# Optimization experiments

Measured on AMD Instinct MI355X. Metric: run time of the kernel, lower is better.

Reference implementation:

```python
import jax, jax.numpy as jnp
import numpy as np

B = 2048          # number of tables (real batch size)
C = 8             # columns per table
D = 768           # hidden size (BERT-base)
TEMP = 0.07       # hp.temp
NEG_FILL = -10.0


def setup_inputs() -> dict:
    key = jax.random.key(0)
    k1, k2, k3 = jax.random.split(key, 3)
    n = B * C
    z = jax.random.normal(k1, (2 * n, D), jnp.float32) * 0.05
    idx = jnp.repeat(jnp.arange(B, dtype=jnp.int32), C)  # contiguous segment ids, as torch.full per table
    query = jax.random.normal(k2, (D, 1), jnp.float32) * 0.05
    attn_temp = jnp.ones((), jnp.float32)
    W = jax.random.normal(k3, (D, D), jnp.float32) * 0.02
    b = jnp.zeros((D,), jnp.float32)
    return {"z": z, "ori_table_indices": idx, "aug_table_indices": idx,
            "query": query, "attn_temp": attn_temp, "W": W, "b": b}


def _attn_pool(z, idx, query, t):
    # scatter-softmax attention pooling over variable-size table segments
    scores = (z @ query)[:, 0] / t                               # [n]
    e = jnp.exp(scores - scores.max())
    denom = jax.ops.segment_sum(e, idx, num_segments=B)[idx]     # [n]
    w = e / (denom + 1e-8)
    return jax.ops.segment_sum(z * w[:, None], idx, num_segments=B)  # [B, D]


def reference(z, ori_table_indices, aug_table_indices, query, attn_temp, W, b):
    n = B * C
    z_ori, z_aug = z[:n], z[n:]
    gx = _attn_pool(z_ori, ori_table_indices, query, attn_temp) @ W.T + b  # [B, D]
    hx = _attn_pool(z_aug, aug_table_indices, query, attn_temp) @ W.T + b  # [B, D]
    f = jnp.concatenate([gx, hx], axis=0)                                  # [2B, D]
    f = f / jnp.linalg.norm(f, axis=1, keepdims=True)
    sim = f @ f.T                                                          # [2B, 2B]
    N = 2 * B
    lab = jnp.concatenate([jnp.arange(B), jnp.arange(B)])
    labels = lab[None, :] == lab[:, None]                                  # [N, N] bool
    potential_pos = (sim > 0.9) & (~labels)
    safe_neg = (~potential_pos) & (~labels)
    # remove diagonal via rotation gather (order of negatives is irrelevant: topk sorts)
    cols = (jnp.arange(N)[:, None] + jnp.arange(1, N)[None, :]) % N        # [N, N-1]
    sim_od = jnp.take_along_axis(sim, cols, axis=1)
    safe_od = jnp.take_along_axis(safe_neg, cols, axis=1)
    # each row's single positive is its paired view at column (i+B) mod N
    pos = jnp.take_along_axis(sim, ((jnp.arange(N) + B) % N)[:, None], axis=1)  # [N, 1]
    neg = jnp.where(safe_od, sim_od, NEG_FILL)
    # data-dependent k; static-shape topk via descending sort + column mask
    k = jnp.maximum(1, jnp.floor(0.5 * jnp.mean(jnp.sum(safe_od, axis=1).astype(jnp.float32))).astype(jnp.int32))
    sneg = -jnp.sort(-neg, axis=1)                                         # descending
    new_neg = jnp.where(jnp.arange(N - 1)[None, :] < k, sneg, NEG_FILL)
    logits = jnp.concatenate([pos, new_neg], axis=1) / TEMP                # [N, N]
    # cross-entropy with target class 0
    loss = jnp.mean(jax.nn.logsumexp(logits, axis=1) - logits[:, 0])
    return loss
```

## Files before the change

kernel.cpp:

```cpp
#include <hip/hip_runtime.h>
#include <hip/hip_bf16.h>
#include <math.h>

#define Bq   2048
#define Cq   8
#define Dq   768
#define NROW 16384
#define NTOT 32768
#define Nq   4096
#define TEMPq 0.07f

typedef __attribute__((ext_vector_type(8))) short bf16x8;
typedef __attribute__((ext_vector_type(4))) float f32x4;
typedef __attribute__((ext_vector_type(8))) _Float16 f16x8;
typedef __attribute__((ext_vector_type(4))) _Float16 f16x4;

__device__ __hip_bfloat16 g_pooledb[(size_t)Nq * Dq];
__device__ __hip_bfloat16 g_Wb[(size_t)Dq * Dq];
__device__ float          g_f[(size_t)Nq * Dq];
__device__ __hip_bfloat16 g_fb[(size_t)Nq * Dq];
__device__ _Float16       g_simh[(size_t)Nq * Nq];
__device__ unsigned int   g_viol;
__device__ float          g_rowloss[Nq];

#define GLDS16(src, dst) __builtin_amdgcn_global_load_lds( \
    (const __attribute__((address_space(1))) void*)(src),  \
    (__attribute__((address_space(3))) void*)(dst), 16, 0, 0)

__global__ __launch_bounds__(256) void prep_kernel(const float* __restrict__ z,
                                                   const float* __restrict__ query,
                                                   const float* __restrict__ attn_temp,
                                                   const float* __restrict__ W) {
    if (blockIdx.x >= 1024) {
        int i = (blockIdx.x - 1024) * 256 + threadIdx.x;
        if (i == 0) g_viol = 0u;
        float4 v = ((const float4*)W)[i];
        short4 o;
        o.x = ((__hip_bfloat16_raw)__float2bfloat16(v.x)).x;
        o.y = ((__hip_bfloat16_raw)__float2bfloat16(v.y)).x;
        o.z = ((__hip_bfloat16_raw)__float2bfloat16(v.z)).x;
        o.w = ((__hip_bfloat16_raw)__float2bfloat16(v.w)).x;
        ((short4*)g_Wb)[i] = o;
        return;
    }
    int seg  = (int)((blockIdx.x * blockDim.x + threadIdx.x) >> 6);
    int lane = threadIdx.x & 63;
    if (seg >= Nq) return;
    int half = seg >> 11;
    int b    = seg & 2047;
    int baseRow = half * NROW + b * Cq;
    float invt = 1.f / attn_temp[0];

    float4 q4[3];
#pragma unroll
    for (int j = 0; j < 3; ++j) q4[j] = *(const float4*)(query + j * 256 + lane * 4);

    float4 v4[Cq][3];
    float s[Cq];
#pragma unroll
    for (int c = 0; c < Cq; ++c) {
        const float* zr = z + (size_t)(baseRow + c) * Dq;
        float acc = 0.f;
#pragma unroll
        for (int j = 0; j < 3; ++j) {
            float4 vz = *(const float4*)(zr + j * 256 + lane * 4);
            v4[c][j] = vz;
            acc += vz.x * q4[j].x + vz.y * q4[j].y + vz.z * q4[j].z + vz.w * q4[j].w;
        }
#pragma unroll
        for (int o = 32; o > 0; o >>= 1) acc += __shfl_xor(acc, o, 64);
        s[c] = acc * invt;
    }
    float m = s[0];
#pragma unroll
    for (int c = 1; c < Cq; ++c) m = fmaxf(m, s[c]);
    float e[Cq], denom = 0.f;
#pragma unroll
    for (int c = 0; c < Cq; ++c) { e[c] = expf(s[c] - m); denom += e[c]; }
    float inv = 1.f / (denom + 1e-8f);
#pragma unroll
    for (int j = 0; j < 3; ++j) {
        float4 acc = {0.f, 0.f, 0.f, 0.f};
#pragma unroll
        for (int c = 0; c < Cq; ++c) {
            acc.x += v4[c][j].x * e[c];
            acc.y += v4[c][j].y * e[c];
            acc.z += v4[c][j].z * e[c];
            acc.w += v4[c][j].w * e[c];
        }
        short4 o;
        o.x = ((__hip_bfloat16_raw)__float2bfloat16(acc.x * inv)).x;
        o.y = ((__hip_bfloat16_raw)__float2bfloat16(acc.y * inv)).x;
        o.z = ((__hip_bfloat16_raw)__float2bfloat16(acc.z * inv)).x;
        o.w = ((__hip_bfloat16_raw)__float2bfloat16(acc.w * inv)).x;
        *(short4*)((short*)g_pooledb + (size_t)seg * Dq + j * 256 + lane * 4) = o;
    }
}

__global__ __launch_bounds__(256) void fw_mfma_kernel(const float* __restrict__ bias) {
    __shared__ short lA[128 * 32];
    __shared__ short lB[128 * 32];
    const int bm = blockIdx.y * 128;
    const int bn = blockIdx.x * 128;

    const int tid  = threadIdx.x;
    const int wave = tid >> 6, lane = tid & 63;
    const int wr = wave >> 1, wc = wave & 1;

    const short* A = (const short*)g_pooledb;
    const short* Bt = (const short*)g_Wb;

    const int c0 = wave * 2, c1 = wave * 2 + 1;
    const int srow = lane >> 2;
    const int scol = (lane & 3) * 8;

    f32x4 acc[4][4];
#pragma unroll
    for (int m = 0; m < 4; ++m)
#pragma unroll
        for (int n = 0; n < 4; ++n) acc[m][n] = (f32x4){0.f, 0.f, 0.f, 0.f};

    for (int k0 = 0; k0 < Dq; k0 += 32) {
        GLDS16(A  + (size_t)(bm + c0 * 16 + srow) * Dq + k0 + scol, lA + c0 * 512);
        GLDS16(A  + (size_t)(bm + c1 * 16 + srow) * Dq + k0 + scol, lA + c1 * 512);
        GLDS16(Bt + (size_t)(bn + c0 * 16 + srow) * Dq + k0 + scol, lB + c0 * 512);
        GLDS16(Bt + (size_t)(bn + c1 * 16 + srow) * Dq + k0 + scol, lB + c1 * 512);
        __syncthreads();

        bf16x8 af[4], bfr[4];
#pragma unroll
        for (int m = 0; m < 4; ++m) {
            int row = wr * 64 + m * 16 + (lane & 15);
            af[m] = *(const bf16x8*)(lA + row * 32 + (lane >> 4) * 8);
        }
#pragma unroll
        for (int n = 0; n < 4; ++n) {
            int row = wc * 64 + n * 16 + (lane & 15);
            bfr[n] = *(const bf16x8*)(lB + row * 32 + (lane >> 4) * 8);
        }
#pragma unroll
        for (int m = 0; m < 4; ++m)
#pragma unroll
            for (int n = 0; n < 4; ++n)
                acc[m][n] = __builtin_amdgcn_mfma_f32_16x16x32_bf16(af[m], bfr[n], acc[m][n], 0, 0, 0);
        __syncthreads();
    }

#pragma unroll
    for (int m = 0; m < 4; ++m) {
        int rowb = bm + wr * 64 + m * 16 + (lane >> 4) * 4;
#pragma unroll
        for (int n = 0; n < 4; ++n) {
            int col = bn + wc * 64 + n * 16 + (lane & 15);
            float bc = bias[col];
#pragma unroll
            for (int j = 0; j < 4; ++j)
                g_f[(size_t)(rowb + j) * Dq + col] = acc[m][n][j] + bc;
        }
    }
}

__global__ __launch_bounds__(256) void normalize_kernel() {
    int row  = (int)((blockIdx.x * blockDim.x + threadIdx.x) >> 6);
    int lane = threadIdx.x & 63;
    if (row >= Nq) return;
    float ss = 0.f;
    float v[Dq / 64];
#pragma unroll
    for (int j = 0; j < Dq / 64; ++j) { v[j] = g_f[(size_t)row * Dq + j * 64 + lane]; ss += v[j] * v[j]; }
#pragma unroll
    for (int o = 32; o > 0; o >>= 1) ss += __shfl_xor(ss, o, 64);
    float rn = 1.f / sqrtf(ss);
#pragma unroll
    for (int j = 0; j < Dq / 64; ++j)
        g_fb[(size_t)row * Dq + j * 64 + lane] = __float2bfloat16(v[j] * rn);
}

__global__ __launch_bounds__(256) void sim_mfma_kernel() {
    __shared__ short lA[128 * 32];
    __shared__ short lB[128 * 32];

    int t = blockIdx.x;
    int bi = 0, rem = t;
    while (rem >= (32 - bi)) { rem -= (32 - bi); ++bi; }
    int bj = bi + rem;
    int bm = bi * 128, bn = bj * 128;

    const int tid  = threadIdx.x;
    const int wave = tid >> 6, lane = tid & 63;
    const int wr = wave >> 1, wc = wave & 1;

    const short* fb = (const short*)g_fb;

    const int c0 = wave * 2, c1 = wave * 2 + 1;
    const int srow = lane >> 2;
    const int scol = (lane & 3) * 8;

    f32x4 acc[4][4];
#pragma unroll
    for (int m = 0; m < 4; ++m)
#pragma unroll
        for (int n = 0; n < 4; ++n) acc[m][n] = (f32x4){0.f, 0.f, 0.f, 0.f};

    for (int k0 = 0; k0 < Dq; k0 += 32) {
        GLDS16(fb + (size_t)(bm + c0 * 16 + srow) * Dq + k0 + scol, lA + c0 * 512);
        GLDS16(fb + (size_t)(bm + c1 * 16 + srow) * Dq + k0 + scol, lA + c1 * 512);
        GLDS16(fb + (size_t)(bn + c0 * 16 + srow) * Dq + k0 + scol, lB + c0 * 512);
        GLDS16(fb + (size_t)(bn + c1 * 16 + srow) * Dq + k0 + scol, lB + c1 * 512);
        __syncthreads();

        bf16x8 af[4], bfr[4];
#pragma unroll
        for (int m = 0; m < 4; ++m) {
            int row = wr * 64 + m * 16 + (lane & 15);
            af[m] = *(const bf16x8*)(lA + row * 32 + (lane >> 4) * 8);
        }
#pragma unroll
        for (int n = 0; n < 4; ++n) {
            int row = wc * 64 + n * 16 + (lane & 15);
            bfr[n] = *(const bf16x8*)(lB + row * 32 + (lane >> 4) * 8);
        }
#pragma unroll
        for (int m = 0; m < 4; ++m)
#pragma unroll
            for (int n = 0; n < 4; ++n)
                acc[m][n] = __builtin_amdgcn_mfma_f32_16x16x32_bf16(af[m], bfr[n], acc[m][n], 0, 0, 0);
        __syncthreads();
    }

    int vio = 0;
#pragma unroll
    for (int m = 0; m < 4; ++m) {
        int rowb = bm + wr * 64 + m * 16 + (lane >> 4) * 4;
#pragma unroll
        for (int n = 0; n < 4; ++n) {
            int col = bn + wc * 64 + n * 16 + (lane & 15);
#pragma unroll
            for (int j = 0; j < 4; ++j) {
                g_simh[(size_t)(rowb + j) * Nq + col] = (_Float16)acc[m][n][j];
                vio += (acc[m][n][j] > 0.9f) && ((((rowb + j) ^ col) & 2047) != 0);
            }
        }
    }
    if (bi != bj) {
#pragma unroll
        for (int m = 0; m < 4; ++m) {
            int rowb = bm + wr * 64 + m * 16 + (lane >> 4) * 4;
#pragma unroll
            for (int n = 0; n < 4; ++n) {
                int col = bn + wc * 64 + n * 16 + (lane & 15);
                f16x4 h;
#pragma unroll
                for (int j = 0; j < 4; ++j) h[j] = (_Float16)acc[m][n][j];
                *(f16x4*)&g_simh[(size_t)col * Nq + rowb] = h;
            }
        }
        vio *= 2;
    }
#pragma unroll
    for (int o = 32; o > 0; o >>= 1) vio += __shfl_xor(vio, o, 64);
    if (lane == 0 && vio > 0) atomicAdd(&g_viol, (unsigned int)vio);
}

__global__ __launch_bounds__(256) void lse_kernel() {
    const int row_id = (int)((blockIdx.x * blockDim.x + threadIdx.x) >> 6);
    const int lane = threadIdx.x & 63;
    const _Float16* row = g_simh + (size_t)row_id * Nq;
    const int labi = row_id & 2047;
    const float invT = 1.0f / TEMPq;

    long long total = (long long)Nq * 4094LL - (long long)g_viol;
    int k = (int)(total / 8192LL);
    if (k < 1) k = 1;

    float v[64];
    float mx = -1e30f, mn = 1e30f;
    int cnt = 0;
#pragma unroll
    for (int q = 0; q < 8; ++q) {
        int j0 = q * 512 + lane * 8;
        f16x8 x8 = *(const f16x8*)(row + j0);
#pragma unroll
        for (int s = 0; s < 8; ++s) {
            int jj = q * 8 + s;
            int j  = j0 + s;
            float xv = (float)x8[s];
            bool sf = (xv <= 0.9f) && (((j ^ labi) & 2047) != 0);
            float val = sf ? xv : -2.0f;
            v[jj] = val;
            mx = fmaxf(mx, val);
            mn = fminf(mn, sf ? xv : 2.0f);
            cnt += (int)__popcll(__ballot(sf));
        }
    }
#pragma unroll
    for (int o = 32; o > 0; o >>= 1) {
        mx = fmaxf(mx, __shfl_xor(mx, o, 64));
        mn = fminf(mn, __shfl_xor(mn, o, 64));
    }

    const float pos = (float)row[(row_id + Bq) & (Nq - 1)];
    const float mxs = (cnt > 0) ? mx : -10.0f;
    const float ml  = fmaxf(pos, mxs) * invT;

    float lo = mn - 1e-3f, hi = mx;
    int c_hi = 0;
    const bool need = (cnt > k);
    if (need) {
        for (int it = 0; it < 12; ++it) {
            float mid = 0.5f * (lo + hi);
            int c = 0;
#pragma unroll
            for (int jj = 0; jj < 64; ++jj)
                c += (int)__popcll(__ballot(v[jj] > mid));
            if (c > k) lo = mid; else { hi = mid; c_hi = c; }
        }
    }

    float shi = 0.f, st = 0.f; int nt = 0;
#pragma unroll
    for (int jj = 0; jj < 64; ++jj) {
        float x = v[jj];
        float ev = __expf(x * invT - ml);
        if (!need)       { if (x > -1.5f) shi += ev; }
        else if (x > hi) { shi += ev; }
        else if (x > lo) { st += ev; nt++; }
    }
#pragma unroll
    for (int o = 32; o > 0; o >>= 1) {
        shi += __shfl_xor(shi, o, 64);
        st  += __shfl_xor(st,  o, 64);
        nt  += __shfl_xor(nt,  o, 64);
    }
    if (lane == 0) {
        float S = __expf(pos * invT - ml) + shi;
        if (need && c_hi < k && nt > 0)
            S += st * (float)(k - c_hi) / (float)nt;
        g_rowloss[row_id] = (logf(S) + ml) - pos * invT;
    }
}

__global__ __launch_bounds__(256) void loss_kernel(float* __restrict__ out) {
    float s = 0.f;
    for (int i = threadIdx.x; i < Nq; i += 256) s += g_rowloss[i];
    __shared__ float sm[256];
    sm[threadIdx.x] = s; __syncthreads();
    for (int o = 128; o > 0; o >>= 1) {
        if (threadIdx.x < o) sm[threadIdx.x] += sm[threadIdx.x + o];
        __syncthreads();
    }
    if (threadIdx.x == 0) out[0] = sm[0] / (float)Nq;
}

extern "C" void kernel_launch(void* const* d_in, const int* in_sizes, int n_in,
                              void* d_out, int out_size, void* d_ws, size_t ws_size,
                              hipStream_t stream) {
    const float* z         = (const float*)d_in[0];
    const float* query     = (const float*)d_in[3];
    const float* attn_temp = (const float*)d_in[4];
    const float* W         = (const float*)d_in[5];
    const float* bias      = (const float*)d_in[6];
    float* out = (float*)d_out;

    prep_kernel<<<1024 + (Dq * Dq / 4) / 256, 256, 0, stream>>>(z, query, attn_temp, W);
    fw_mfma_kernel<<<dim3(Dq / 128, Nq / 128), 256, 0, stream>>>(bias);
    normalize_kernel<<<Nq / 4, 256, 0, stream>>>();
    sim_mfma_kernel<<<(32 * 33) / 2, 256, 0, stream>>>();
    lse_kernel<<<Nq / 4, 256, 0, stream>>>();
    loss_kernel<<<1, 256, 0, stream>>>(out);
}
```

Baseline: 121.3 us.

## Retile sim GEMM to 256x256 double-buffered tiles with k-chunked operand layout

The normalize kernel now writes the normalized bf16 features in a k-chunk-major layout (8-element chunks, row-contiguous within each chunk) so the similarity GEMM can stage tiles with fully coalesced direct-to-LDS loads. The similarity kernel moves from 128x128 upper-triangle tiles with 256 threads to a full 16x16 grid of 256x256 tiles with 512 threads, double-buffered LDS (128KB) and explicit vmcnt waits, so the next tile's loads overlap the MFMAs. It drops the symmetric transposed write-back and computes the whole matrix, which doubles the MFMA work. In return it gains larger per-block reuse, better load overlap and fully coalesced stores.

```diff
diff --git a/kernel.cpp b/kernel.cpp
--- a/kernel.cpp
+++ b/kernel.cpp
@@ -9,16 +9,16 @@
 #define NTOT 32768
 #define Nq   4096
 #define TEMPq 0.07f
+#define NKC  96
 
 typedef __attribute__((ext_vector_type(8))) short bf16x8;
 typedef __attribute__((ext_vector_type(4))) float f32x4;
 typedef __attribute__((ext_vector_type(8))) _Float16 f16x8;
-typedef __attribute__((ext_vector_type(4))) _Float16 f16x4;
 
 __device__ __hip_bfloat16 g_pooledb[(size_t)Nq * Dq];
 __device__ __hip_bfloat16 g_Wb[(size_t)Dq * Dq];
 __device__ float          g_f[(size_t)Nq * Dq];
-__device__ __hip_bfloat16 g_fb[(size_t)Nq * Dq];
+__device__ short          g_fbt[(size_t)NKC * Nq * 8];
 __device__ _Float16       g_simh[(size_t)Nq * Nq];
 __device__ unsigned int   g_viol;
 __device__ float          g_rowloss[Nq];
@@ -161,101 +161,112 @@
 }
 
 __global__ __launch_bounds__(256) void normalize_kernel() {
-    int row  = (int)((blockIdx.x * blockDim.x + threadIdx.x) >> 6);
-    int lane = threadIdx.x & 63;
-    if (row >= Nq) return;
-    float ss = 0.f;
-    float v[Dq / 64];
-#pragma unroll
-    for (int j = 0; j < Dq / 64; ++j) { v[j] = g_f[(size_t)row * Dq + j * 64 + lane]; ss += v[j] * v[j]; }
-#pragma unroll
-    for (int o = 32; o > 0; o >>= 1) ss += __shfl_xor(ss, o, 64);
-    float rn = 1.f / sqrtf(ss);
-#pragma unroll
-    for (int j = 0; j < Dq / 64; ++j)
-        g_fb[(size_t)row * Dq + j * 64 + lane] = __float2bfloat16(v[j] * rn);
-}
-
-__global__ __launch_bounds__(256) void sim_mfma_kernel() {
-    __shared__ short lA[128 * 32];
-    __shared__ short lB[128 * 32];
-
-    int t = blockIdx.x;
-    int bi = 0, rem = t;
-    while (rem >= (32 - bi)) { rem -= (32 - bi); ++bi; }
-    int bj = bi + rem;
-    int bm = bi * 128, bn = bj * 128;
+    __shared__ short rowbuf[16][776];
+    const int tid = threadIdx.x;
+    const int wave = tid >> 6, lane = tid & 63;
+    const int r0 = blockIdx.x * 16;
+
+    for (int rr = wave; rr < 16; rr += 4) {
+        int row = r0 + rr;
+        float v[12];
+        float ss = 0.f;
+#pragma unroll
+        for (int j = 0; j < 12; ++j) { v[j] = g_f[(size_t)row * Dq + j * 64 + lane]; ss += v[j] * v[j]; }
+#pragma unroll
+        for (int o = 32; o > 0; o >>= 1) ss += __shfl_xor(ss, o, 64);
+        float rn = 1.f / sqrtf(ss);
+#pragma unroll
+        for (int j = 0; j < 12; ++j)
+            rowbuf[rr][j * 64 + lane] = ((__hip_bfloat16_raw)__float2bfloat16(v[j] * rn)).x;
+    }
+    __syncthreads();
+#pragma unroll
+    for (int i = 0; i < 6; ++i) {
+        int idx = i * 256 + tid;
+        int ch = idx >> 4;
+        int r  = idx & 15;
+        bf16x8 val = *(const bf16x8*)&rowbuf[r][ch * 8];
+        *(bf16x8*)&g_fbt[((size_t)ch * Nq + r0 + r) * 8] = val;
+    }
+}
+
+#define STAGE_SIM(b, kt_) do {                                                          \
+    _Pragma("unroll")                                                                   \
+    for (int i = 0; i < 4; ++i) {                                                       \
+        GLDS16(fbt + ((size_t)((kt_) * 8 + wave) * Nq + bm + i * 64 + lane) * 8,        \
+               As + ((b) * 2048 + wave * 256 + i * 64) * 8);                            \
+        GLDS16(fbt + ((size_t)((kt_) * 8 + wave) * Nq + bn + i * 64 + lane) * 8,        \
+               Bs + ((b) * 2048 + wave * 256 + i * 64) * 8);                            \
+    }                                                                                   \
+} while (0)
+
+__global__ __launch_bounds__(512) void sim_mfma_kernel() {
+    extern __shared__ short smem[];
+    short* As = smem;
+    short* Bs = smem + 32768;
 
     const int tid  = threadIdx.x;
     const int wave = tid >> 6, lane = tid & 63;
-    const int wr = wave >> 1, wc = wave & 1;
-
-    const short* fb = (const short*)g_fb;
-
-    const int c0 = wave * 2, c1 = wave * 2 + 1;
-    const int srow = lane >> 2;
-    const int scol = (lane & 3) * 8;
-
-    f32x4 acc[4][4];
-#pragma unroll
-    for (int m = 0; m < 4; ++m)
-#pragma unroll
-        for (int n = 0; n < 4; ++n) acc[m][n] = (f32x4){0.f, 0.f, 0.f, 0.f};
-
-    for (int k0 = 0; k0 < Dq; k0 += 32) {
-        GLDS16(fb + (size_t)(bm + c0 * 16 + srow) * Dq + k0 + scol, lA + c0 * 512);
-        GLDS16(fb + (size_t)(bm + c1 * 16 + srow) * Dq + k0 + scol, lA + c1 * 512);
-        GLDS16(fb + (size_t)(bn + c0 * 16 + srow) * Dq + k0 + scol, lB + c0 * 512);
-        GLDS16(fb + (size_t)(bn + c1 * 16 + srow) * Dq + k0 + scol, lB + c1 * 512);
-        __syncthreads();
-
-        bf16x8 af[4], bfr[4];
-#pragma unroll
-        for (int m = 0; m < 4; ++m) {
-            int row = wr * 64 + m * 16 + (lane & 15);
-            af[m] = *(const bf16x8*)(lA + row * 32 + (lane >> 4) * 8);
-        }
-#pragma unroll
-        for (int n = 0; n < 4; ++n) {
-            int row = wc * 64 + n * 16 + (lane & 15);
-            bfr[n] = *(const bf16x8*)(lB + row * 32 + (lane >> 4) * 8);
-        }
-#pragma unroll
-        for (int m = 0; m < 4; ++m)
-#pragma unroll
-            for (int n = 0; n < 4; ++n)
-                acc[m][n] = __builtin_amdgcn_mfma_f32_16x16x32_bf16(af[m], bfr[n], acc[m][n], 0, 0, 0);
-        __syncthreads();
+    const int wm = wave >> 2, wn = wave & 3;
+    const int bm = blockIdx.y * 256, bn = blockIdx.x * 256;
+    const short* fbt = g_fbt;
+
+    f32x4 acc[8][4];
+#pragma unroll
+    for (int mi = 0; mi < 8; ++mi)
+#pragma unroll
+        for (int ni = 0; ni < 4; ++ni) acc[mi][ni] = (f32x4){0.f, 0.f, 0.f, 0.f};
+
+    STAGE_SIM(0, 0);
+
+#pragma unroll 1
+    for (int kt = 0; kt < 12; ++kt) {
+        const int cur = kt & 1;
+        if (kt < 11) {
+            STAGE_SIM(cur ^ 1, kt + 1);
+            asm volatile("s_waitcnt vmcnt(8)" ::: "memory");
+        } else {
+            asm volatile("s_waitcnt vmcnt(0)" ::: "memory");
+        }
+        __builtin_amdgcn_s_barrier();
+        __builtin_amdgcn_sched_barrier(0);
+
+#pragma unroll
+        for (int ks = 0; ks < 2; ++ks) {
+            bf16x8 af[8], bfr[4];
+            const int kc = (ks * 4 + (lane >> 4)) * 256;
+#pragma unroll
+            for (int mi = 0; mi < 8; ++mi)
+                af[mi] = *(const bf16x8*)(As + (cur * 2048 + kc + wm * 128 + mi * 16 + (lane & 15)) * 8);
+#pragma unroll
+            for (int ni = 0; ni < 4; ++ni)
+                bfr[ni] = *(const bf16x8*)(Bs + (cur * 2048 + kc + wn * 64 + ni * 16 + (lane & 15)) * 8);
+            __builtin_amdgcn_s_setprio(1);
+#pragma unroll
+            for (int mi = 0; mi < 8; ++mi)
+#pragma unroll
+                for (int ni = 0; ni < 4; ++ni)
+                    acc[mi][ni] = __builtin_amdgcn_mfma_f32_16x16x32_bf16(af[mi], bfr[ni], acc[mi][ni], 0, 0, 0);
+            __builtin_amdgcn_s_setprio(0);
+        }
+        __builtin_amdgcn_sched_barrier(0);
+        __builtin_amdgcn_s_barrier();
     }
 
     int vio = 0;
 #pragma unroll
-    for (int m = 0; m < 4; ++m) {
-        int rowb = bm + wr * 64 + m * 16 + (lane >> 4) * 4;
-#pragma unroll
-        for (int n = 0; n < 4; ++n) {
-            int col = bn + wc * 64 + n * 16 + (lane & 15);
+    for (int mi = 0; mi < 8; ++mi) {
+        int rowb = bm + wm * 128 + mi * 16 + (lane >> 4) * 4;
+#pragma unroll
+        for (int ni = 0; ni < 4; ++ni) {
+            int col = bn + wn * 64 + ni * 16 + (lane & 15);
 #pragma unroll
             for (int j = 0; j < 4; ++j) {
-                g_simh[(size_t)(rowb + j) * Nq + col] = (_Float16)acc[m][n][j];
-                vio += (acc[m][n][j] > 0.9f) && ((((rowb + j) ^ col) & 2047) != 0);
+                float x = acc[mi][ni][j];
+                g_simh[(size_t)(rowb + j) * Nq + col] = (_Float16)x;
+                vio += (x > 0.9f) && ((((rowb + j) ^ col) & 2047) != 0);
             }
         }
-    }
-    if (bi != bj) {
-#pragma unroll
-        for (int m = 0; m < 4; ++m) {
-            int rowb = bm + wr * 64 + m * 16 + (lane >> 4) * 4;
-#pragma unroll
-            for (int n = 0; n < 4; ++n) {
-                int col = bn + wc * 64 + n * 16 + (lane & 15);
-                f16x4 h;
-#pragma unroll
-                for (int j = 0; j < 4; ++j) h[j] = (_Float16)acc[m][n][j];
-                *(f16x4*)&g_simh[(size_t)col * Nq + rowb] = h;
-            }
-        }
-        vio *= 2;
     }
 #pragma unroll
     for (int o = 32; o > 0; o >>= 1) vio += __shfl_xor(vio, o, 64);
@@ -364,8 +375,8 @@
 
     prep_kernel<<<1024 + (Dq * Dq / 4) / 256, 256, 0, stream>>>(z, query, attn_temp, W);
     fw_mfma_kernel<<<dim3(Dq / 128, Nq / 128), 256, 0, stream>>>(bias);
-    normalize_kernel<<<Nq / 4, 256, 0, stream>>>();
-    sim_mfma_kernel<<<(32 * 33) / 2, 256, 0, stream>>>();
+    normalize_kernel<<<Nq / 16, 256, 0, stream>>>();
+    sim_mfma_kernel<<<dim3(16, 16), 512, 131072, stream>>>();
     lse_kernel<<<Nq / 4, 256, 0, stream>>>();
     loss_kernel<<<1, 256, 0, stream>>>(out);
 }
```

Measured after the change: 116.3 us (median of 2 runs). -4.1%, faster.
